# Optimization experiments

Hardware: AMD Instinct MI355X
Metric: run time of the kernel (lower is better)

Reference implementation:

```python
import jax, jax.numpy as jnp
import numpy as np

# Static pyramid config (must match setup_inputs' source_shape / level_start)
LEVEL_SHAPES = [(100, 100), (50, 50), (25, 25), (13, 13)]
DIM = 256
N_HEAD = 8
HEAD_DIM = DIM // N_HEAD
N_LEVEL = 4
N_POINT = 4
DIM_FF = 1024
B = 8
Q = 2048
LEN_IN = sum(h * w for h, w in LEVEL_SHAPES)


def layer_norm(x, g, b, eps=1e-5):
    m = jnp.mean(x, axis=-1, keepdims=True)
    v = jnp.mean(jnp.square(x - m), axis=-1, keepdims=True)
    return (x - m) * jax.lax.rsqrt(v + eps) * g + b


def bilinear_sample(v_flat, loc, H, W):
    # v_flat: (BH, H*W, hd); loc: (BH, Q, P, 2) normalized [0,1] as (x, y)
    # grid_sample align_corners=False with zero padding: pixel = loc*size - 0.5
    x = loc[..., 0] * W - 0.5
    y = loc[..., 1] * H - 0.5
    x0 = jnp.floor(x)
    y0 = jnp.floor(y)
    wx = (x - x0)[..., None]
    wy = (y - y0)[..., None]
    x0i = x0.astype(jnp.int32)
    y0i = y0.astype(jnp.int32)

    def gather(xi, yi):
        valid = ((xi >= 0) & (xi < W) & (yi >= 0) & (yi < H)).astype(v_flat.dtype)
        idx = jnp.clip(yi, 0, H - 1) * W + jnp.clip(xi, 0, W - 1)  # (BH,Q,P)
        BH, Qq, P = idx.shape
        f = jnp.take_along_axis(v_flat, idx.reshape(BH, Qq * P, 1), axis=1)
        return f.reshape(BH, Qq, P, -1) * valid[..., None]

    g00 = gather(x0i, y0i)
    g01 = gather(x0i + 1, y0i)
    g10 = gather(x0i, y0i + 1)
    g11 = gather(x0i + 1, y0i + 1)
    top = g00 * (1.0 - wx) + g01 * wx
    bot = g10 * (1.0 - wx) + g11 * wx
    return top * (1.0 - wy) + bot * wy


def ms_deform_attn_core(value, loc, attn):
    # value: (B, Lin, nh, hd); loc: (B, Q, nh, L, P, 2); attn: (B, Q, nh, L, P)
    Bv, Lin, nh, hd = value.shape
    Qq = loc.shape[1]
    out = jnp.zeros((Bv * nh, Qq, hd), value.dtype)
    start = 0
    for l, (H, W) in enumerate(LEVEL_SHAPES):
        v = value[:, start:start + H * W]                       # (B, HW, nh, hd)
        v = v.transpose(0, 2, 1, 3).reshape(Bv * nh, H * W, hd)
        ll = loc[:, :, :, l].transpose(0, 2, 1, 3, 4).reshape(Bv * nh, Qq, N_POINT, 2)
        aa = attn[:, :, :, l].transpose(0, 2, 1, 3).reshape(Bv * nh, Qq, N_POINT, 1)
        samp = bilinear_sample(v, ll, H, W)                     # (B*nh, Q, P, hd)
        out = out + jnp.sum(samp * aa, axis=2)
        start += H * W
    return out.reshape(Bv, nh, Qq, hd).transpose(0, 2, 1, 3).reshape(Bv, Qq, nh * hd)


def setup_inputs() -> dict:
    key = jax.random.key(0)
    ks = jax.random.split(key, 24)
    std = 0.02
    inp = {
        'input': jax.random.normal(ks[0], (B, Q, DIM), jnp.float32),
        'pos': jax.random.normal(ks[1], (B, Q, DIM), jnp.float32),
        'reference_point': jax.random.uniform(ks[2], (B, Q, N_LEVEL, 2), jnp.float32),
        'source': jax.random.normal(ks[3], (B, LEN_IN, DIM), jnp.float32),
        'source_shape': jnp.array(LEVEL_SHAPES, jnp.int64),
        'level_start': jnp.array(np.cumsum([0] + [h * w for h, w in LEVEL_SHAPES[:-1]]), jnp.int64),
        'source_mask': jnp.zeros((B, LEN_IN), jnp.bool_),
        # LayerNorms
        'ln1_g': jnp.ones((DIM,), jnp.float32), 'ln1_b': jnp.zeros((DIM,), jnp.float32),
        'ln2_g': jnp.ones((DIM,), jnp.float32), 'ln2_b': jnp.zeros((DIM,), jnp.float32),
        # MSDeformAttn projections
        'Wv': std * jax.random.normal(ks[4], (DIM, DIM), jnp.float32), 'bv': jnp.zeros((DIM,), jnp.float32),
        'Woff': std * jax.random.normal(ks[5], (DIM, N_HEAD * N_LEVEL * N_POINT * 2), jnp.float32),
        'boff': 0.5 * jax.random.normal(ks[6], (N_HEAD * N_LEVEL * N_POINT * 2,), jnp.float32),
        'Wattn': std * jax.random.normal(ks[7], (DIM, N_HEAD * N_LEVEL * N_POINT), jnp.float32),
        'battn': jnp.zeros((N_HEAD * N_LEVEL * N_POINT,), jnp.float32),
        'Wout': std * jax.random.normal(ks[8], (DIM, DIM), jnp.float32), 'bout': jnp.zeros((DIM,), jnp.float32),
        # FFN
        'W1': std * jax.random.normal(ks[9], (DIM, DIM_FF), jnp.float32), 'b1': jnp.zeros((DIM_FF,), jnp.float32),
        'W2': std * jax.random.normal(ks[10], (DIM_FF, DIM), jnp.float32), 'b2': jnp.zeros((DIM,), jnp.float32),
    }
    return inp


def reference(input, pos, reference_point, source, source_shape, level_start, source_mask,
              ln1_g, ln1_b, ln2_g, ln2_b, Wv, bv, Woff, boff, Wattn, battn, Wout, bout,
              W1, b1, W2, b2):
    # ---- cross norm + pos ----
    q = layer_norm(input, ln1_g, ln1_b)
    qp = q + pos
    # ---- MSDeformAttn ----
    value = source @ Wv + bv
    value = jnp.where(source_mask[..., None], 0.0, value)
    value = value.reshape(B, LEN_IN, N_HEAD, HEAD_DIM)
    offsets = (qp @ Woff + boff).reshape(B, Q, N_HEAD, N_LEVEL, N_POINT, 2)
    attn = (qp @ Wattn + battn).reshape(B, Q, N_HEAD, N_LEVEL * N_POINT)
    attn = jax.nn.softmax(attn, axis=-1).reshape(B, Q, N_HEAD, N_LEVEL, N_POINT)
    # offset normalizer is (W, H) per level
    normalizer = jnp.array([[w, h] for h, w in LEVEL_SHAPES], jnp.float32)
    loc = reference_point[:, :, None, :, None, :] + offsets / normalizer[None, None, None, :, None, :]
    out = ms_deform_attn_core(value, loc, attn)
    out = out @ Wout + bout
    x = input + out  # dropout is identity in eval
    # ---- FFN ----
    h = layer_norm(x, ln2_g, ln2_b)
    h = jax.nn.relu(h @ W1 + b1) @ W2 + b2
    x = x + h
    return (x, loc)
```

## Files before the change

### kernel.cpp

```cpp
#include <hip/hip_runtime.h>
#include <hip/hip_bf16.h>
#include <cstdint>
#include <cstddef>

#define B_    8
#define Q_    2048
#define DIM_  256
#define NH    8
#define HD    32
#define NL    4
#define NP    4
#define DFF   1024
#define LEN_IN_ 13294
#define MV    (B_*LEN_IN_)
#define MVPAD 106368
#define MQ    (B_*Q_)

typedef unsigned short u16;
typedef unsigned int   u32;
typedef __attribute__((ext_vector_type(8))) short short8;
typedef __attribute__((ext_vector_type(4))) float f32x4v;
typedef __attribute__((ext_vector_type(4))) unsigned short u16x4;

static __device__ __forceinline__ u16 f2bf(float f){
  union { float f; unsigned u; } x; x.f = f;
  unsigned r = x.u + 0x7fffu + ((x.u >> 16) & 1u);
  return (u16)(r >> 16);
}

template<int EPI, bool AF32>
__global__ __launch_bounds__(256)
void gemm_k(const void* __restrict__ Ap, const u16* __restrict__ Bt,
            const float* __restrict__ bias, const float* __restrict__ res,
            void* __restrict__ outp, int N, int K, int Mstore)
{
  __shared__ u16 As[128*64];
  __shared__ u16 Bs[128*64];
  const int t = threadIdx.x;
  const int l = t & 63, wid = t >> 6;
  const int wm = wid >> 1, wn = wid & 1;
  const int m0 = blockIdx.x * 128, n0 = blockIdx.y * 128;

  f32x4v acc[4][4];
#pragma unroll
  for (int i = 0; i < 4; ++i)
#pragma unroll
    for (int j = 0; j < 4; ++j) acc[i][j] = 0.f;

  const int nkt = K >> 6;
  for (int kt = 0; kt < nkt; ++kt) {
#pragma unroll
    for (int i = 0; i < 4; ++i) {
      int chunk = i * 256 + t;
      int row   = chunk >> 3;
      int c16   = chunk & 7;
      int sc    = c16 ^ (row & 7);
      if (AF32) {
        const int gr = m0 + row;
        float4 f0 = {0.f,0.f,0.f,0.f}, f1 = {0.f,0.f,0.f,0.f};
        if (gr < Mstore) {
          const float* ga = (const float*)Ap + (size_t)gr * K + kt * 64 + sc * 8;
          f0 = *reinterpret_cast<const float4*>(ga);
          f1 = *reinterpret_cast<const float4*>(ga + 4);
        }
        short8 pk;
        pk[0]=(short)f2bf(f0.x); pk[1]=(short)f2bf(f0.y); pk[2]=(short)f2bf(f0.z); pk[3]=(short)f2bf(f0.w);
        pk[4]=(short)f2bf(f1.x); pk[5]=(short)f2bf(f1.y); pk[6]=(short)f2bf(f1.z); pk[7]=(short)f2bf(f1.w);
        *reinterpret_cast<short8*>(As + chunk * 8) = pk;
      } else {
        const u16* ga = (const u16*)Ap + (size_t)(m0 + row) * K + kt * 64 + sc * 8;
        __builtin_amdgcn_global_load_lds((const __attribute__((address_space(1))) void*)ga,
                                         (__attribute__((address_space(3))) void*)(As + chunk * 8), 16, 0, 0);
      }
      const u16* gb = Bt + (size_t)(n0 + row) * K + kt * 64 + sc * 8;
      __builtin_amdgcn_global_load_lds((const __attribute__((address_space(1))) void*)gb,
                                       (__attribute__((address_space(3))) void*)(Bs + chunk * 8), 16, 0, 0);
    }
    __syncthreads();
#pragma unroll
    for (int kk = 0; kk < 2; ++kk) {
      short8 af[4], bfr[4];
      const int lr  = l & 15;
      const int c   = kk * 4 + (l >> 4);
      const int swz = c ^ (lr & 7);
#pragma unroll
      for (int mi = 0; mi < 4; ++mi) {
        int r = wm * 64 + mi * 16 + lr;
        af[mi] = *reinterpret_cast<const short8*>(As + (r * 8 + swz) * 8);
      }
#pragma unroll
      for (int ni = 0; ni < 4; ++ni) {
        int r = wn * 64 + ni * 16 + lr;
        bfr[ni] = *reinterpret_cast<const short8*>(Bs + (r * 8 + swz) * 8);
      }
#pragma unroll
      for (int mi = 0; mi < 4; ++mi)
#pragma unroll
        for (int ni = 0; ni < 4; ++ni)
          acc[mi][ni] = __builtin_amdgcn_mfma_f32_16x16x32_bf16(af[mi], bfr[ni], acc[mi][ni], 0, 0, 0);
    }
    __syncthreads();
  }

  const int lr4 = l >> 4;
#pragma unroll
  for (int mi = 0; mi < 4; ++mi) {
    int rowb = m0 + wm * 64 + mi * 16 + lr4 * 4;
#pragma unroll
    for (int ni = 0; ni < 4; ++ni) {
      int col = n0 + wn * 64 + ni * 16 + (l & 15);
      float bb = bias[col];
#pragma unroll
      for (int v = 0; v < 4; ++v) {
        int r = rowb + v;
        if (r < Mstore) {
          float cv = acc[mi][ni][v] + bb;
          if (EPI == 2) cv += res[(size_t)r * N + col];
          if (EPI == 3) cv = fmaxf(cv, 0.f);
          if (EPI == 0 || EPI == 2) ((float*)outp)[(size_t)r * N + col] = cv;
          else                      ((u16*)outp)[(size_t)r * N + col] = f2bf(cv);
        }
      }
    }
  }
}

__global__ void prep_weights(const float* __restrict__ Wv,   const float* __restrict__ Woff,
                             const float* __restrict__ Wattn,const float* __restrict__ Wout,
                             const float* __restrict__ W1,   const float* __restrict__ W2,
                             const float* __restrict__ boff, const float* __restrict__ battn,
                             u16* __restrict__ WvT, u16* __restrict__ WcombT,
                             u16* __restrict__ WoutT, u16* __restrict__ W1T,
                             u16* __restrict__ W2T, float* __restrict__ bcomb)
{
  const int gid = blockIdx.x * 256 + threadIdx.x;
  const int R0 = 65536, R1 = R0 + 98304, R2 = R1 + 65536, R3 = R2 + 262144,
            R4 = R3 + 262144, R5 = R4 + 384;
  if (gid < R0) {
    int n = gid >> 8, k = gid & 255;
    WvT[gid] = f2bf(Wv[(size_t)k * 256 + n]);
  } else if (gid < R1) {
    int lo = gid - R0, n = lo >> 8, k = lo & 255;
    float s = (n < 256) ? Woff[(size_t)k * 256 + n] : Wattn[(size_t)k * 128 + (n - 256)];
    WcombT[lo] = f2bf(s);
  } else if (gid < R2) {
    int lo = gid - R1, n = lo >> 8, k = lo & 255;
    WoutT[lo] = f2bf(Wout[(size_t)k * 256 + n]);
  } else if (gid < R3) {
    int lo = gid - R2, n = lo >> 8, k = lo & 255;
    W1T[lo] = f2bf(W1[(size_t)k * 1024 + n]);
  } else if (gid < R4) {
    int lo = gid - R3, n = lo >> 10, k = lo & 1023;
    W2T[lo] = f2bf(W2[(size_t)k * 256 + n]);
  } else if (gid < R5) {
    int lo = gid - R4;
    bcomb[lo] = (lo < 256) ? boff[lo] : battn[lo - 256];
  }
}

template<bool ADDPOS>
__global__ __launch_bounds__(256)
void ln_k(const float* __restrict__ x, const float* __restrict__ pos,
          const float* __restrict__ g, const float* __restrict__ b, u16* __restrict__ out)
{
  const int warp = threadIdx.x >> 6, l = threadIdx.x & 63;
  const int row = blockIdx.x * 4 + warp;
  const float4 xv = reinterpret_cast<const float4*>(x + (size_t)row * 256)[l];
  float s = xv.x + xv.y + xv.z + xv.w;
#pragma unroll
  for (int o = 32; o; o >>= 1) s += __shfl_xor(s, o);
  const float mean = s * (1.f / 256.f);
  const float d0 = xv.x - mean, d1 = xv.y - mean, d2 = xv.z - mean, d3 = xv.w - mean;
  float vs = d0 * d0 + d1 * d1 + d2 * d2 + d3 * d3;
#pragma unroll
  for (int o = 32; o; o >>= 1) vs += __shfl_xor(vs, o);
  const float rs = rsqrtf(vs * (1.f / 256.f) + 1e-5f);
  const float4 gv = reinterpret_cast<const float4*>(g)[l];
  const float4 bv = reinterpret_cast<const float4*>(b)[l];
  float o0 = d0 * rs * gv.x + bv.x;
  float o1 = d1 * rs * gv.y + bv.y;
  float o2 = d2 * rs * gv.z + bv.z;
  float o3 = d3 * rs * gv.w + bv.w;
  if (ADDPOS) {
    const float4 pv = reinterpret_cast<const float4*>(pos + (size_t)row * 256)[l];
    o0 += pv.x; o1 += pv.y; o2 += pv.z; o3 += pv.w;
  }
  u16x4 ov; ov.x = f2bf(o0); ov.y = f2bf(o1); ov.z = f2bf(o2); ov.w = f2bf(o3);
  reinterpret_cast<u16x4*>(out + (size_t)row * 256)[l] = ov;
}

__global__ __launch_bounds__(256)
void msdeform_k(const u16* __restrict__ value, const float* __restrict__ oa,
                const float* __restrict__ refpt, float* __restrict__ locout,
                u16* __restrict__ outp)
{
  const int t = threadIdx.x;
  const int rloc = t >> 7;
  const int rem = t & 127;
  const int h = rem >> 4, p = rem & 15;
  const int row = blockIdx.x * 2 + rloc;
  const int b = row >> 11;
  const int lv = p >> 2;
  const float* orow = oa + (size_t)row * 384;

  const float araw = orow[256 + h * 16 + p];
  float mx = araw;
#pragma unroll
  for (int o = 1; o < 16; o <<= 1) mx = fmaxf(mx, __shfl_xor(mx, o, 16));
  const float e = __expf(araw - mx);
  float se = e;
#pragma unroll
  for (int o = 1; o < 16; o <<= 1) se += __shfl_xor(se, o, 16);
  const float aw = e / se;

  const float2 off = *reinterpret_cast<const float2*>(orow + h * 32 + p * 2);
  const float rn = (lv == 0) ? (1.f / 100.f) : (lv == 1) ? (1.f / 50.f)
                 : (lv == 2) ? (1.f / 25.f) : (1.f / 13.f);
  const float rx = refpt[(size_t)row * 8 + lv * 2 + 0];
  const float ry = refpt[(size_t)row * 8 + lv * 2 + 1];
  const float lx = rx + off.x * rn;
  const float ly = ry + off.y * rn;
  float2 lw; lw.x = lx; lw.y = ly;
  *reinterpret_cast<float2*>(locout + (((size_t)row * 8 + h) * 16 + p) * 2) = lw;

  const int Wl = (lv == 0) ? 100 : (lv == 1) ? 50 : (lv == 2) ? 25 : 13;
  const int st = (lv == 0) ? 0 : (lv == 1) ? 10000 : (lv == 2) ? 12500 : 13125;
  const float Wf = (float)Wl;
  const float xx = lx * Wf - 0.5f, yy = ly * Wf - 0.5f;
  const float xf = floorf(xx), yf = floorf(yy);
  const float wx = xx - xf, wy = yy - yf;
  const int x0 = (int)xf, y0 = (int)yf;
  const int xc0 = min(max(x0, 0), Wl - 1), xc1 = min(max(x0 + 1, 0), Wl - 1);
  const int yc0 = min(max(y0, 0), Wl - 1), yc1 = min(max(y0 + 1, 0), Wl - 1);
  const float vx0 = (x0 >= 0 && x0 < Wl) ? 1.f : 0.f;
  const float vx1 = (x0 + 1 >= 0 && x0 + 1 < Wl) ? 1.f : 0.f;
  const float vy0 = (y0 >= 0 && y0 < Wl) ? 1.f : 0.f;
  const float vy1 = (y0 + 1 >= 0 && y0 + 1 < Wl) ? 1.f : 0.f;
  const int o00 = st + yc0 * Wl + xc0, o01 = st + yc0 * Wl + xc1;
  const int o10 = st + yc1 * Wl + xc0, o11 = st + yc1 * Wl + xc1;
  const float w00 = aw * (1.f - wx) * (1.f - wy) * vx0 * vy0;
  const float w01 = aw * wx * (1.f - wy) * vx1 * vy0;
  const float w10 = aw * (1.f - wx) * wy * vx0 * vy1;
  const float w11 = aw * wx * wy * vx1 * vy1;

  const char* vbase = (const char*)value + (size_t)b * LEN_IN_ * 512 + (size_t)(h * 32 + p * 2) * 2;
  float a0 = 0.f, a1 = 0.f;
#pragma unroll
  for (int q = 0; q < 16; ++q) {
    const int   c00 = __shfl(o00, q, 16), c01 = __shfl(o01, q, 16);
    const int   c10 = __shfl(o10, q, 16), c11 = __shfl(o11, q, 16);
    const float u00 = __shfl(w00, q, 16), u01 = __shfl(w01, q, 16);
    const float u10 = __shfl(w10, q, 16), u11 = __shfl(w11, q, 16);
    const u32 g00 = *reinterpret_cast<const u32*>(vbase + (size_t)c00 * 512);
    const u32 g01 = *reinterpret_cast<const u32*>(vbase + (size_t)c01 * 512);
    const u32 g10 = *reinterpret_cast<const u32*>(vbase + (size_t)c10 * 512);
    const u32 g11 = *reinterpret_cast<const u32*>(vbase + (size_t)c11 * 512);
    union { u32 u; float f; } lo, hi;
    lo.u = g00 << 16; hi.u = g00 & 0xffff0000u; a0 += u00 * lo.f; a1 += u00 * hi.f;
    lo.u = g01 << 16; hi.u = g01 & 0xffff0000u; a0 += u01 * lo.f; a1 += u01 * hi.f;
    lo.u = g10 << 16; hi.u = g10 & 0xffff0000u; a0 += u10 * lo.f; a1 += u10 * hi.f;
    lo.u = g11 << 16; hi.u = g11 & 0xffff0000u; a0 += u11 * lo.f; a1 += u11 * hi.f;
  }
  const u32 res = ((u32)f2bf(a1) << 16) | (u32)f2bf(a0);
  reinterpret_cast<u32*>(outp)[(size_t)row * 128 + h * 16 + p] = res;
}

extern "C" void kernel_launch(void* const* d_in, const int* in_sizes, int n_in,
                              void* d_out, int out_size, void* d_ws, size_t ws_size,
                              hipStream_t stream)
{
  (void)in_sizes; (void)n_in; (void)out_size; (void)ws_size;
  const float* input  = (const float*)d_in[0];
  const float* pos    = (const float*)d_in[1];
  const float* refpt  = (const float*)d_in[2];
  const float* source = (const float*)d_in[3];
  const float* ln1_g  = (const float*)d_in[7];
  const float* ln1_b  = (const float*)d_in[8];
  const float* ln2_g  = (const float*)d_in[9];
  const float* ln2_b  = (const float*)d_in[10];
  const float* Wv     = (const float*)d_in[11];
  const float* bv     = (const float*)d_in[12];
  const float* Woff   = (const float*)d_in[13];
  const float* boff   = (const float*)d_in[14];
  const float* Wattn  = (const float*)d_in[15];
  const float* battn  = (const float*)d_in[16];
  const float* Wout   = (const float*)d_in[17];
  const float* bout   = (const float*)d_in[18];
  const float* W1     = (const float*)d_in[19];
  const float* b1     = (const float*)d_in[20];
  const float* W2     = (const float*)d_in[21];
  const float* b2     = (const float*)d_in[22];

  char* ws = (char*)d_ws;
  u16*   WvT    = (u16*)  (ws + 0);
  u16*   WcombT = (u16*)  (ws + 131072);
  u16*   WoutT  = (u16*)  (ws + 327680);
  u16*   W1T    = (u16*)  (ws + 458752);
  u16*   W2T    = (u16*)  (ws + 983040);
  float* bcomb  = (float*)(ws + 1507328);
  u16*   valueB = (u16*)  (ws + 1508864);
  u16*   hB     = (u16*)  (ws + 1508864);
  u16*   qpB    = (u16*)  (ws + 55969280);
  u16*   msout  = (u16*)  (ws + 55969280);
  float* oa     = (float*)(ws + 64357888);
  float* xbuf   = (float*)(ws + 89523712);
  u16*   xnB    = (u16*)  (ws + 106300928);

  float* out_x   = (float*)d_out;
  float* out_loc = (float*)d_out + (size_t)MQ * DIM_;

  hipLaunchKernelGGL(prep_weights, dim3(2946), dim3(256), 0, stream,
                     Wv, Woff, Wattn, Wout, W1, W2, boff, battn,
                     WvT, WcombT, WoutT, W1T, W2T, bcomb);

  hipLaunchKernelGGL((ln_k<true>), dim3(MQ / 4), dim3(256), 0, stream, input, pos, ln1_g, ln1_b, qpB);

  hipLaunchKernelGGL((gemm_k<1, true>), dim3(MVPAD / 128, 2), dim3(256), 0, stream,
                     (const void*)source, WvT, bv, (const float*)nullptr, (void*)valueB, 256, 256, MV);

  hipLaunchKernelGGL((gemm_k<0, false>), dim3(MQ / 128, 3), dim3(256), 0, stream,
                     (const void*)qpB, WcombT, bcomb, (const float*)nullptr, (void*)oa, 384, 256, MQ);

  hipLaunchKernelGGL(msdeform_k, dim3(MQ / 2), dim3(256), 0, stream,
                     valueB, oa, refpt, out_loc, msout);

  hipLaunchKernelGGL((gemm_k<2, false>), dim3(MQ / 128, 2), dim3(256), 0, stream,
                     (const void*)msout, WoutT, bout, input, (void*)xbuf, 256, 256, MQ);

  hipLaunchKernelGGL((ln_k<false>), dim3(MQ / 4), dim3(256), 0, stream, xbuf, (const float*)nullptr, ln2_g, ln2_b, xnB);

  hipLaunchKernelGGL((gemm_k<3, false>), dim3(MQ / 128, DFF / 128), dim3(256), 0, stream,
                     (const void*)xnB, W1T, b1, (const float*)nullptr, (void*)hB, DFF, 256, MQ);

  hipLaunchKernelGGL((gemm_k<2, false>), dim3(MQ / 128, 2), dim3(256), 0, stream,
                     (const void*)hB, W2T, b2, xbuf, (void*)out_x, 256, 1024, MQ);
}
```

Before: 430.6 us.

## Double-buffer GEMM LDS tiles to overlap next-tile loads with MFMA

Gives the shared GEMM kernel two LDS buffers for A and B and prefetches the next K tile while MFMAs run on the current one. For fp32 A inputs, the next tile is held in registers and converted to bf16 after the compute step. This drops one barrier per K step and hides global load latency. The cost is double the LDS footprint (64 KB per block) and more registers, which may reduce occupancy.

```diff
diff --git a/kernel.cpp b/kernel.cpp
--- a/kernel.cpp
+++ b/kernel.cpp
@@ -28,14 +28,18 @@
   return (u16)(r >> 16);
 }
 
+#define GLDS(gp, lp) __builtin_amdgcn_global_load_lds( \
+    (const __attribute__((address_space(1))) void*)(gp), \
+    (__attribute__((address_space(3))) void*)(lp), 16, 0, 0)
+
 template<int EPI, bool AF32>
 __global__ __launch_bounds__(256)
 void gemm_k(const void* __restrict__ Ap, const u16* __restrict__ Bt,
             const float* __restrict__ bias, const float* __restrict__ res,
             void* __restrict__ outp, int N, int K, int Mstore)
 {
-  __shared__ u16 As[128*64];
-  __shared__ u16 Bs[128*64];
+  __shared__ u16 As[2][128*64];
+  __shared__ u16 Bs[2][128*64];
   const int t = threadIdx.x;
   const int l = t & 63, wid = t >> 6;
   const int wm = wid >> 1, wn = wid & 1;
@@ -48,35 +52,74 @@
     for (int j = 0; j < 4; ++j) acc[i][j] = 0.f;
 
   const int nkt = K >> 6;
-  for (int kt = 0; kt < nkt; ++kt) {
+
+  {
+    float4 pa[8];
 #pragma unroll
     for (int i = 0; i < 4; ++i) {
-      int chunk = i * 256 + t;
-      int row   = chunk >> 3;
-      int c16   = chunk & 7;
-      int sc    = c16 ^ (row & 7);
+      const int chunk = i * 256 + t;
+      const int row = chunk >> 3;
+      const int sc = (chunk & 7) ^ (row & 7);
       if (AF32) {
         const int gr = m0 + row;
-        float4 f0 = {0.f,0.f,0.f,0.f}, f1 = {0.f,0.f,0.f,0.f};
+        float4 z = {0.f, 0.f, 0.f, 0.f};
+        pa[2*i] = z; pa[2*i+1] = z;
         if (gr < Mstore) {
-          const float* ga = (const float*)Ap + (size_t)gr * K + kt * 64 + sc * 8;
-          f0 = *reinterpret_cast<const float4*>(ga);
-          f1 = *reinterpret_cast<const float4*>(ga + 4);
+          const float* ga = (const float*)Ap + (size_t)gr * K + sc * 8;
+          pa[2*i]   = *reinterpret_cast<const float4*>(ga);
+          pa[2*i+1] = *reinterpret_cast<const float4*>(ga + 4);
         }
+      } else {
+        const u16* ga = (const u16*)Ap + (size_t)(m0 + row) * K + sc * 8;
+        GLDS(ga, As[0] + chunk * 8);
+      }
+      const u16* gb = Bt + (size_t)(n0 + row) * K + sc * 8;
+      GLDS(gb, Bs[0] + chunk * 8);
+    }
+    asm volatile("s_waitcnt vmcnt(0)" ::: "memory");
+    if (AF32) {
+#pragma unroll
+      for (int i = 0; i < 4; ++i) {
+        const int chunk = i * 256 + t;
         short8 pk;
-        pk[0]=(short)f2bf(f0.x); pk[1]=(short)f2bf(f0.y); pk[2]=(short)f2bf(f0.z); pk[3]=(short)f2bf(f0.w);
-        pk[4]=(short)f2bf(f1.x); pk[5]=(short)f2bf(f1.y); pk[6]=(short)f2bf(f1.z); pk[7]=(short)f2bf(f1.w);
-        *reinterpret_cast<short8*>(As + chunk * 8) = pk;
-      } else {
-        const u16* ga = (const u16*)Ap + (size_t)(m0 + row) * K + kt * 64 + sc * 8;
-        __builtin_amdgcn_global_load_lds((const __attribute__((address_space(1))) void*)ga,
-                                         (__attribute__((address_space(3))) void*)(As + chunk * 8), 16, 0, 0);
-      }
-      const u16* gb = Bt + (size_t)(n0 + row) * K + kt * 64 + sc * 8;
-      __builtin_amdgcn_global_load_lds((const __attribute__((address_space(1))) void*)gb,
-                                       (__attribute__((address_space(3))) void*)(Bs + chunk * 8), 16, 0, 0);
+        pk[0]=(short)f2bf(pa[2*i].x);   pk[1]=(short)f2bf(pa[2*i].y);
+        pk[2]=(short)f2bf(pa[2*i].z);   pk[3]=(short)f2bf(pa[2*i].w);
+        pk[4]=(short)f2bf(pa[2*i+1].x); pk[5]=(short)f2bf(pa[2*i+1].y);
+        pk[6]=(short)f2bf(pa[2*i+1].z); pk[7]=(short)f2bf(pa[2*i+1].w);
+        *reinterpret_cast<short8*>(As[0] + chunk * 8) = pk;
+      }
     }
     __syncthreads();
+  }
+
+  int cur = 0;
+  for (int kt = 0; kt < nkt; ++kt) {
+    const bool pf = (kt + 1 < nkt);
+    float4 pa[8];
+    if (pf) {
+      const int kn = (kt + 1) * 64;
+#pragma unroll
+      for (int i = 0; i < 4; ++i) {
+        const int chunk = i * 256 + t;
+        const int row = chunk >> 3;
+        const int sc = (chunk & 7) ^ (row & 7);
+        if (AF32) {
+          const int gr = m0 + row;
+          float4 z = {0.f, 0.f, 0.f, 0.f};
+          pa[2*i] = z; pa[2*i+1] = z;
+          if (gr < Mstore) {
+            const float* ga = (const float*)Ap + (size_t)gr * K + kn + sc * 8;
+            pa[2*i]   = *reinterpret_cast<const float4*>(ga);
+            pa[2*i+1] = *reinterpret_cast<const float4*>(ga + 4);
+          }
+        } else {
+          const u16* ga = (const u16*)Ap + (size_t)(m0 + row) * K + kn + sc * 8;
+          GLDS(ga, As[cur ^ 1] + chunk * 8);
+        }
+        const u16* gb = Bt + (size_t)(n0 + row) * K + kn + sc * 8;
+        GLDS(gb, Bs[cur ^ 1] + chunk * 8);
+      }
+    }
 #pragma unroll
     for (int kk = 0; kk < 2; ++kk) {
       short8 af[4], bfr[4];
@@ -86,12 +129,12 @@
 #pragma unroll
       for (int mi = 0; mi < 4; ++mi) {
         int r = wm * 64 + mi * 16 + lr;
-        af[mi] = *reinterpret_cast<const short8*>(As + (r * 8 + swz) * 8);
+        af[mi] = *reinterpret_cast<const short8*>(As[cur] + (r * 8 + swz) * 8);
       }
 #pragma unroll
       for (int ni = 0; ni < 4; ++ni) {
         int r = wn * 64 + ni * 16 + lr;
-        bfr[ni] = *reinterpret_cast<const short8*>(Bs + (r * 8 + swz) * 8);
+        bfr[ni] = *reinterpret_cast<const short8*>(Bs[cur] + (r * 8 + swz) * 8);
       }
 #pragma unroll
       for (int mi = 0; mi < 4; ++mi)
@@ -99,7 +142,23 @@
         for (int ni = 0; ni < 4; ++ni)
           acc[mi][ni] = __builtin_amdgcn_mfma_f32_16x16x32_bf16(af[mi], bfr[ni], acc[mi][ni], 0, 0, 0);
     }
+    if (pf) {
+      asm volatile("s_waitcnt vmcnt(0)" ::: "memory");
+      if (AF32) {
+#pragma unroll
+        for (int i = 0; i < 4; ++i) {
+          const int chunk = i * 256 + t;
+          short8 pk;
+          pk[0]=(short)f2bf(pa[2*i].x);   pk[1]=(short)f2bf(pa[2*i].y);
+          pk[2]=(short)f2bf(pa[2*i].z);   pk[3]=(short)f2bf(pa[2*i].w);
+          pk[4]=(short)f2bf(pa[2*i+1].x); pk[5]=(short)f2bf(pa[2*i+1].y);
+          pk[6]=(short)f2bf(pa[2*i+1].z); pk[7]=(short)f2bf(pa[2*i+1].w);
+          *reinterpret_cast<short8*>(As[cur ^ 1] + chunk * 8) = pk;
+        }
+      }
+    }
     __syncthreads();
+    cur ^= 1;
   }
 
   const int lr4 = l >> 4;
```

Measured after the change: 429.1 us. No clear change (-0.3%).
